# Performance work log

Measured on AMD Instinct MI355X. Metric: run time of the kernel, lower is better.

Reference implementation:

```python
import jax, jax.numpy as jnp
import numpy as np
import math

NUM_HEADS = 16
HEAD_DIM = 64
D_MODEL = NUM_HEADS * HEAD_DIM  # 1024
B, S = 4, 2048

def setup_inputs() -> dict:
    key = jax.random.key(0)
    ks = jax.random.split(key, 8)
    sd = 1.0 / math.sqrt(D_MODEL)
    return {
        "hidden_states": jax.random.normal(ks[0], (B, S, D_MODEL), jnp.float32),
        "attention_mask": jnp.zeros((B, 1, 1, S), jnp.float32),
        "Wq": jax.random.normal(ks[1], (D_MODEL, D_MODEL), jnp.float32) * sd,
        "bq": jnp.zeros((D_MODEL,), jnp.float32),
        "Wk": jax.random.normal(ks[2], (D_MODEL, D_MODEL), jnp.float32) * sd,
        "bk": jnp.zeros((D_MODEL,), jnp.float32),
        "Wv": jax.random.normal(ks[3], (D_MODEL, D_MODEL), jnp.float32) * sd,
        "bv": jnp.zeros((D_MODEL,), jnp.float32),
    }

def _split_heads(x):
    # [B, S, D] -> [B, H, S, hd]
    b, s, _ = x.shape
    return x.reshape(b, s, NUM_HEADS, HEAD_DIM).transpose(0, 2, 1, 3)

def reference(hidden_states, attention_mask, Wq, bq, Wk, bk, Wv, bv):
    # Linear projections (torch nn.Linear: x @ W.T + b)
    q = _split_heads(hidden_states @ Wq.T + bq)
    k = _split_heads(hidden_states @ Wk.T + bk)
    v = _split_heads(hidden_states @ Wv.T + bv)
    scale = 1.0 / math.sqrt(HEAD_DIM)
    # [B, H, Sq, Sk] attention scores, fully materialized as in the original
    scores = jnp.einsum("bhqd,bhkd->bhqk", q, k) * scale + attention_mask
    # relusq replacement for softmax
    probs = jnp.square(jax.nn.relu(scores))
    ctx = jnp.einsum("bhqk,bhkd->bhqd", probs, v)  # [B, H, S, hd]
    b = ctx.shape[0]
    return ctx.transpose(0, 2, 1, 3).reshape(b, -1, D_MODEL)
```

## Files before the change

### kernel.cpp

```cpp
#include <hip/hip_runtime.h>


typedef __bf16 bf16x8 __attribute__((ext_vector_type(8)));
typedef __bf16 bf16x4 __attribute__((ext_vector_type(4)));
typedef __bf16 bf16x2 __attribute__((ext_vector_type(2)));
typedef short  s16x4  __attribute__((ext_vector_type(4)));
typedef float  f32x4  __attribute__((ext_vector_type(4)));
typedef float  f32x16 __attribute__((ext_vector_type(16)));
typedef float  floatx4 __attribute__((ext_vector_type(4)));
typedef unsigned u32x2 __attribute__((ext_vector_type(2)));
typedef unsigned u32x4 __attribute__((ext_vector_type(4)));

#define MFMA16(a, b, c) __builtin_amdgcn_mfma_f32_16x16x32_bf16(a, b, c, 0, 0, 0)
#define MFMA32(a, b, c) __builtin_amdgcn_mfma_f32_32x32x16_bf16(a, b, c, 0, 0, 0)

#define WAITCNT_VM0() __builtin_amdgcn_s_waitcnt(0x0F70)
#define BARRIER() __builtin_amdgcn_s_barrier()
#define SETPRIO(p) __builtin_amdgcn_s_setprio(p)

__device__ __forceinline__ void glds16(const __bf16* g, __bf16* l) {
    __builtin_amdgcn_global_load_lds(
        (const __attribute__((address_space(1))) void*)g,
        (__attribute__((address_space(3))) void*)l, 16, 0, 0);
}

__global__ __launch_bounds__(256) void convert_kernel(
    const float* __restrict__ X, const float* __restrict__ Wq,
    const float* __restrict__ Wk, const float* __restrict__ Wv,
    __bf16* __restrict__ Xb, __bf16* __restrict__ Wqb,
    __bf16* __restrict__ Wkb, __bf16* __restrict__ Wvb)
{
    int blk = blockIdx.x;
    const float* src; __bf16* dst; size_t base;
    if (blk < 4096)      { src = X;  dst = Xb;  base = (size_t)blk * 2048; }
    else if (blk < 4608) { src = Wq; dst = Wqb; base = (size_t)(blk - 4096) * 2048; }
    else if (blk < 5120) { src = Wk; dst = Wkb; base = (size_t)(blk - 4608) * 2048; }
    else                 { src = Wv; dst = Wvb; base = (size_t)(blk - 5120) * 2048; }
    size_t off = base + (size_t)threadIdx.x * 8;
    floatx4 a = *(const floatx4*)(src + off);
    floatx4 c = *(const floatx4*)(src + off + 4);
    bf16x8 o;
    o[0] = (__bf16)a[0]; o[1] = (__bf16)a[1]; o[2] = (__bf16)a[2]; o[3] = (__bf16)a[3];
    o[4] = (__bf16)c[0]; o[5] = (__bf16)c[1]; o[6] = (__bf16)c[2]; o[7] = (__bf16)c[3];
    *(bf16x8*)(dst + off) = o;
}

__global__ __launch_bounds__(256) void qkv_gemm_kernel(
    const __bf16* __restrict__ Xb,
    const __bf16* __restrict__ Wqb, const __bf16* __restrict__ Wkb,
    const __bf16* __restrict__ Wvb,
    const float* __restrict__ bq, const float* __restrict__ bk,
    const float* __restrict__ bv,
    __bf16* __restrict__ qws, __bf16* __restrict__ kws, __bf16* __restrict__ vws)
{
    __shared__ __bf16 As[2][128 * 64];
    __shared__ __bf16 Bs[2][128 * 64];

    const int tid  = threadIdx.x;
    const int lane = tid & 63;
    const int wave = tid >> 6;
    const int wm   = (wave >> 1) * 64;
    const int wn   = (wave & 1) * 64;
    const int quad = lane >> 4;
    const int l16  = lane & 15;
    const int m0   = blockIdx.y * 128;

    const int sel = blockIdx.x >> 3;
    const bool vmode = (sel == 2);
    const __bf16* Wb = (sel == 0) ? Wqb : (sel == 1) ? Wkb : Wvb;
    const float* bias = (sel == 0) ? bq : (sel == 1) ? bk : bv;
    __bf16* outp = (sel == 0) ? qws : (sel == 1) ? kws : vws;
    const int n0 = (blockIdx.x & 7) * 128;

    const int woffA = vmode ? wm : wn;
    const int woffB = vmode ? wn : wm;

    const int srow = lane >> 3;
    const int schk = lane & 7;

    f32x4 acc[4][4] = {};

    #pragma unroll
    for (int i = 0; i < 4; ++i) {
        int rb = wave * 32 + i * 8;
        int r  = rb + srow;
        int c  = schk ^ (r & 7);
        glds16(Xb + (size_t)(m0 + r) * 1024 + c * 8, &As[0][rb * 64]);
        glds16(Wb + (size_t)(n0 + r) * 1024 + c * 8, &Bs[0][rb * 64]);
    }
    WAITCNT_VM0();
    BARRIER();

    for (int s = 0; s < 16; ++s) {
        const int kn = ((s + 1) & 15) * 64;
        const int nb = (s + 1) & 1;
        const int bc = s & 1;
        #pragma unroll
        for (int i = 0; i < 4; ++i) {
            int rb = wave * 32 + i * 8;
            int r  = rb + srow;
            int c  = schk ^ (r & 7);
            glds16(Xb + (size_t)(m0 + r) * 1024 + kn + c * 8, &As[nb][rb * 64]);
            glds16(Wb + (size_t)(n0 + r) * 1024 + kn + c * 8, &Bs[nb][rb * 64]);
        }

        const __bf16* Pa_ = vmode ? &As[bc][0] : &Bs[bc][0];
        const __bf16* Pb_ = vmode ? &Bs[bc][0] : &As[bc][0];

        SETPRIO(1);
        #pragma unroll
        for (int kk8 = 0; kk8 < 8; kk8 += 4) {
            bf16x8 af[4], bfr[4];
            #pragma unroll
            for (int a = 0; a < 4; ++a)
                af[a] = *(const bf16x8*)&Pa_[(woffA + a * 16 + l16) * 64 +
                                             (((kk8 + quad) ^ (l16 & 7)) * 8)];
            #pragma unroll
            for (int bb = 0; bb < 4; ++bb)
                bfr[bb] = *(const bf16x8*)&Pb_[(woffB + bb * 16 + l16) * 64 +
                                               (((kk8 + quad) ^ (l16 & 7)) * 8)];
            #pragma unroll
            for (int a = 0; a < 4; ++a)
                #pragma unroll
                for (int bb = 0; bb < 4; ++bb)
                    acc[a][bb] = MFMA16(af[a], bfr[bb], acc[a][bb]);
        }
        SETPRIO(0);

        WAITCNT_VM0();
        BARRIER();
    }

    if (!vmode) {
        #pragma unroll
        for (int a = 0; a < 4; ++a) {
            int n = n0 + woffA + a * 16 + quad * 4;
            floatx4 bv4 = *(const floatx4*)&bias[n];
            int h = n >> 6, d0 = n & 63;
            #pragma unroll
            for (int bb = 0; bb < 4; ++bb) {
                int m = m0 + woffB + bb * 16 + l16;
                int bt = m >> 11, ss = m & 2047;
                bf16x4 o;
                #pragma unroll
                for (int r = 0; r < 4; ++r)
                    o[r] = (__bf16)(acc[a][bb][r] + bv4[r]);
                *(bf16x4*)&outp[((size_t)(bt * 16 + h) * 2048 + ss) * 64 + d0] = o;
            }
        }
    } else {
        #pragma unroll
        for (int a = 0; a < 4; ++a) {
            int m = m0 + woffA + a * 16 + quad * 4;
            int bt = m >> 11, s0 = m & 2047;
            #pragma unroll
            for (int bb = 0; bb < 4; ++bb) {
                int n = n0 + woffB + bb * 16 + l16;
                float bvv = bias[n];
                int h = n >> 6, d = n & 63;
                bf16x4 o;
                #pragma unroll
                for (int r = 0; r < 4; ++r)
                    o[r] = (__bf16)(acc[a][bb][r] + bvv);
                *(bf16x4*)&outp[((size_t)(bt * 16 + h) * 64 + d) * 2048 + s0] = o;
            }
        }
    }
}

__global__ __launch_bounds__(512, 4) void attn_kernel(
    const __bf16* __restrict__ Q, const __bf16* __restrict__ K,
    const __bf16* __restrict__ Vt, const float* __restrict__ mask,
    float* __restrict__ out)
{
    __shared__ __bf16 Ks[2][2][64 * 64];
    __shared__ __bf16 Vs[2][2][64 * 64];
    __shared__ float  Ms[2048];

    const int tid  = threadIdx.x;
    const int lane = tid & 63;
    const int wave = tid >> 6;
    const int l32  = lane & 31;
    const int hi   = lane >> 5;
    const int bh   = blockIdx.x;
    const int b    = bh >> 4;
    const int h    = bh & 15;
    const int q0w  = blockIdx.y * 256 + wave * 32;

    const __bf16* Qb = Q  + (size_t)bh * 2048 * 64;
    const __bf16* Kb = K  + (size_t)bh * 2048 * 64;
    const __bf16* Vb = Vt + (size_t)bh * 64 * 2048;
    const float*  mb = mask + b * 2048;

    const int rb = wave * 8;
    const int sr = rb + (lane >> 3);
    const int sc = ((lane & 7) ^ (sr & 7)) * 8;

    bf16x8 aq[4];
    #pragma unroll
    for (int dk = 0; dk < 4; ++dk)
        aq[dk] = *(const bf16x8*)(Qb +
            (size_t)(q0w + l32) * 64 + dk * 16 + hi * 8);

    f32x16 co0 = {}, co1 = {};

    glds16(Kb + (size_t)sr * 64 + sc,        &Ks[0][0][rb * 64]);
    glds16(Kb + (size_t)(64 + sr) * 64 + sc, &Ks[0][1][rb * 64]);
    glds16(Vb + (size_t)sr * 2048 + sc,      &Vs[0][0][rb * 64]);
    glds16(Vb + (size_t)sr * 2048 + 64 + sc, &Vs[0][1][rb * 64]);
    glds16((const __bf16*)mb + (size_t)wave * 512 + lane * 8,
           (__bf16*)Ms + wave * 512);
    WAITCNT_VM0();
    BARRIER();

    for (int t = 0; t < 16; ++t) {
        const int kn = ((t + 1) & 15) * 128;
        const int nb = (t + 1) & 1;
        const int cb = t & 1;
        glds16(Kb + (size_t)(kn + sr) * 64 + sc,       &Ks[nb][0][rb * 64]);
        glds16(Kb + (size_t)(kn + 64 + sr) * 64 + sc,  &Ks[nb][1][rb * 64]);
        glds16(Vb + (size_t)sr * 2048 + kn + sc,       &Vs[nb][0][rb * 64]);
        glds16(Vb + (size_t)sr * 2048 + kn + 64 + sc,  &Vs[nb][1][rb * 64]);

        #pragma unroll
        for (int hf = 0; hf < 2; ++hf) {
            const __bf16* Kt = &Ks[cb][hf][0];
            const __bf16* Vtl = &Vs[cb][hf][0];
            const int k0 = t * 128 + hf * 64;

            f32x16 st0 = {}, st1 = {};
            SETPRIO(1);
            #pragma unroll
            for (int dk = 0; dk < 4; ++dk) {
                const int g = dk * 2 + hi;
                const int c0 = (g ^ (l32 & 7)) * 8;
                bf16x8 ak0 = *(const bf16x8*)&Kt[l32 * 64 + c0];
                bf16x8 ak1 = *(const bf16x8*)&Kt[(32 + l32) * 64 + c0];
                st0 = MFMA32(ak0, aq[dk], st0);
                st1 = MFMA32(ak1, aq[dk], st1);
            }
            SETPRIO(0);

            #pragma unroll
            for (int kg = 0; kg < 2; ++kg) {
                const f32x16 s = kg ? st1 : st0;
                const f32x4 zero4 = {};
                unsigned W[4][2];
                #pragma unroll
                for (int G = 0; G < 4; ++G) {
                    f32x4 v;
                    v[0] = s[G * 4 + 0]; v[1] = s[G * 4 + 1];
                    v[2] = s[G * 4 + 2]; v[3] = s[G * 4 + 3];
                    f32x4 mk = *(const f32x4*)&Ms[k0 + kg * 32 + G * 8 + hi * 4];
                    v = v * 0.125f + mk;
                    v = __builtin_elementwise_max(v, zero4);
                    v = v * v;
                    bf16x2 w0, w1;
                    w0[0] = (__bf16)v[0]; w0[1] = (__bf16)v[1];
                    w1[0] = (__bf16)v[2]; w1[1] = (__bf16)v[3];
                    W[G][0] = __builtin_bit_cast(unsigned, w0);
                    W[G][1] = __builtin_bit_cast(unsigned, w1);
                }
                u32x2 s00 = __builtin_amdgcn_permlane32_swap(W[0][0], W[1][0], false, false);
                u32x2 s01 = __builtin_amdgcn_permlane32_swap(W[0][1], W[1][1], false, false);
                u32x2 s10 = __builtin_amdgcn_permlane32_swap(W[2][0], W[3][0], false, false);
                u32x2 s11 = __builtin_amdgcn_permlane32_swap(W[2][1], W[3][1], false, false);
                u32x4 f0, f1;
                f0[0] = s00[0]; f0[1] = s01[0]; f0[2] = s00[1]; f0[3] = s01[1];
                f1[0] = s10[0]; f1[1] = s11[0]; f1[2] = s10[1]; f1[3] = s11[1];
                bf16x8 pa0 = __builtin_bit_cast(bf16x8, f0);
                bf16x8 pa1 = __builtin_bit_cast(bf16x8, f1);

                SETPRIO(1);
                #pragma unroll
                for (int dt = 0; dt < 2; ++dt) {
                    const int d = dt * 32 + l32;
                    const int ch0 = (kg * 4 + hi) ^ (d & 7);
                    const int ch1 = (kg * 4 + 2 + hi) ^ (d & 7);
                    bf16x8 vb0 = *(const bf16x8*)&Vtl[d * 64 + ch0 * 8];
                    bf16x8 vb1 = *(const bf16x8*)&Vtl[d * 64 + ch1 * 8];
                    if (dt == 0) {
                        co0 = MFMA32(pa0, vb0, co0);
                        co0 = MFMA32(pa1, vb1, co0);
                    } else {
                        co1 = MFMA32(pa0, vb0, co1);
                        co1 = MFMA32(pa1, vb1, co1);
                    }
                }
                SETPRIO(0);
            }
        }

        WAITCNT_VM0();
        BARRIER();
    }

    #pragma unroll
    for (int r = 0; r < 16; ++r) {
        int q = q0w + (r & 3) + 8 * (r >> 2) + 4 * hi;
        float* orow = &out[(((size_t)b * 2048 + q) * 16 + h) * 64];
        orow[l32]      = co0[r];
        orow[32 + l32] = co1[r];
    }
}

extern "C" void kernel_launch(void* const* d_in, const int* in_sizes, int n_in,
                              void* d_out, int out_size, void* d_ws, size_t ws_size,
                              hipStream_t stream) {
    const float* hidden = (const float*)d_in[0];
    const float* mask   = (const float*)d_in[1];
    const float* Wq     = (const float*)d_in[2];
    const float* bq     = (const float*)d_in[3];
    const float* Wk     = (const float*)d_in[4];
    const float* bk     = (const float*)d_in[5];
    const float* Wv     = (const float*)d_in[6];
    const float* bv     = (const float*)d_in[7];
    float* out = (float*)d_out;

    __bf16* qws = (__bf16*)d_ws;
    __bf16* kws = qws + (size_t)64 * 2048 * 64;
    __bf16* vws = kws + (size_t)64 * 2048 * 64;
    __bf16* Xb  = vws + (size_t)64 * 2048 * 64;
    __bf16* Wqb = Xb  + (size_t)8192 * 1024;
    __bf16* Wkb = Wqb + (size_t)1024 * 1024;
    __bf16* Wvb = Wkb + (size_t)1024 * 1024;

    convert_kernel<<<dim3(5632), dim3(256), 0, stream>>>(hidden, Wq, Wk, Wv,
                                                         Xb, Wqb, Wkb, Wvb);
    qkv_gemm_kernel<<<dim3(24, 64), dim3(256), 0, stream>>>(Xb, Wqb, Wkb, Wvb,
                                                            bq, bk, bv,
                                                            qws, kws, vws);
    attn_kernel<<<dim3(64, 8), dim3(512), 0, stream>>>(qws, kws, vws, mask, out);
}
```

Measured before the change: 241.3 us.

## Shrink attention blocks to 4 waves with 64-key tiles and more blocks

The attention kernel now uses 256-thread blocks covering 128 queries, and processes keys in 64-wide tiles over 32 iterations instead of 128-wide tiles over 16. Launching 1024 blocks instead of 512 and using half the shared memory for K/V buffers is meant to improve occupancy and load balance across CUs. In exchange, each K/V tile is reused by fewer query waves, so global/L2 traffic for K and V doubles, and there are twice as many barriers per block.

After: 241.0 us. Within noise of the previous version (-0.1%).

```diff
diff --git a/kernel.cpp b/kernel.cpp
--- a/kernel.cpp
+++ b/kernel.cpp
@@ -168,13 +168,13 @@
     }
 }
 
-__global__ __launch_bounds__(512, 4) void attn_kernel(
+__global__ __launch_bounds__(256, 4) void attn_kernel(
     const __bf16* __restrict__ Q, const __bf16* __restrict__ K,
     const __bf16* __restrict__ Vt, const float* __restrict__ mask,
     float* __restrict__ out)
 {
-    __shared__ __bf16 Ks[2][2][64 * 64];
-    __shared__ __bf16 Vs[2][2][64 * 64];
+    __shared__ __bf16 Ks[2][64 * 64];
+    __shared__ __bf16 Vs[2][64 * 64];
     __shared__ float  Ms[2048];
 
     const int tid  = threadIdx.x;
@@ -185,14 +185,14 @@
     const int bh   = blockIdx.x;
     const int b    = bh >> 4;
     const int h    = bh & 15;
-    const int q0w  = blockIdx.y * 256 + wave * 32;
+    const int q0w  = blockIdx.y * 128 + wave * 32;
 
     const __bf16* Qb = Q  + (size_t)bh * 2048 * 64;
     const __bf16* Kb = K  + (size_t)bh * 2048 * 64;
     const __bf16* Vb = Vt + (size_t)bh * 64 * 2048;
     const float*  mb = mask + b * 2048;
 
-    const int rb = wave * 8;
+    const int rb = wave * 16;
     const int sr = rb + (lane >> 3);
     const int sc = ((lane & 7) ^ (sr & 7)) * 8;
 
@@ -204,91 +204,90 @@
 
     f32x16 co0 = {}, co1 = {};
 
-    glds16(Kb + (size_t)sr * 64 + sc,        &Ks[0][0][rb * 64]);
-    glds16(Kb + (size_t)(64 + sr) * 64 + sc, &Ks[0][1][rb * 64]);
-    glds16(Vb + (size_t)sr * 2048 + sc,      &Vs[0][0][rb * 64]);
-    glds16(Vb + (size_t)sr * 2048 + 64 + sc, &Vs[0][1][rb * 64]);
-    glds16((const __bf16*)mb + (size_t)wave * 512 + lane * 8,
-           (__bf16*)Ms + wave * 512);
+    glds16(Kb + (size_t)sr * 64 + sc,            &Ks[0][rb * 64]);
+    glds16(Kb + (size_t)(sr + 8) * 64 + sc,      &Ks[0][(rb + 8) * 64]);
+    glds16(Vb + (size_t)sr * 2048 + sc,          &Vs[0][rb * 64]);
+    glds16(Vb + (size_t)(sr + 8) * 2048 + sc,    &Vs[0][(rb + 8) * 64]);
+    glds16((const __bf16*)mb + (size_t)(wave * 2) * 512 + lane * 8,
+           (__bf16*)Ms + (wave * 2) * 512);
+    glds16((const __bf16*)mb + (size_t)(wave * 2 + 1) * 512 + lane * 8,
+           (__bf16*)Ms + (wave * 2 + 1) * 512);
     WAITCNT_VM0();
     BARRIER();
 
-    for (int t = 0; t < 16; ++t) {
-        const int kn = ((t + 1) & 15) * 128;
+    for (int t = 0; t < 32; ++t) {
+        const int kn = ((t + 1) & 31) * 64;
         const int nb = (t + 1) & 1;
         const int cb = t & 1;
-        glds16(Kb + (size_t)(kn + sr) * 64 + sc,       &Ks[nb][0][rb * 64]);
-        glds16(Kb + (size_t)(kn + 64 + sr) * 64 + sc,  &Ks[nb][1][rb * 64]);
-        glds16(Vb + (size_t)sr * 2048 + kn + sc,       &Vs[nb][0][rb * 64]);
-        glds16(Vb + (size_t)sr * 2048 + kn + 64 + sc,  &Vs[nb][1][rb * 64]);
-
-        #pragma unroll
-        for (int hf = 0; hf < 2; ++hf) {
-            const __bf16* Kt = &Ks[cb][hf][0];
-            const __bf16* Vtl = &Vs[cb][hf][0];
-            const int k0 = t * 128 + hf * 64;
-
-            f32x16 st0 = {}, st1 = {};
+        glds16(Kb + (size_t)(kn + sr) * 64 + sc,         &Ks[nb][rb * 64]);
+        glds16(Kb + (size_t)(kn + sr + 8) * 64 + sc,     &Ks[nb][(rb + 8) * 64]);
+        glds16(Vb + (size_t)sr * 2048 + kn + sc,         &Vs[nb][rb * 64]);
+        glds16(Vb + (size_t)(sr + 8) * 2048 + kn + sc,   &Vs[nb][(rb + 8) * 64]);
+
+        const __bf16* Kt = &Ks[cb][0];
+        const __bf16* Vtl = &Vs[cb][0];
+        const int k0 = t * 64;
+
+        f32x16 st0 = {}, st1 = {};
+        SETPRIO(1);
+        #pragma unroll
+        for (int dk = 0; dk < 4; ++dk) {
+            const int g = dk * 2 + hi;
+            const int c0 = (g ^ (l32 & 7)) * 8;
+            bf16x8 ak0 = *(const bf16x8*)&Kt[l32 * 64 + c0];
+            bf16x8 ak1 = *(const bf16x8*)&Kt[(32 + l32) * 64 + c0];
+            st0 = MFMA32(ak0, aq[dk], st0);
+            st1 = MFMA32(ak1, aq[dk], st1);
+        }
+        SETPRIO(0);
+
+        #pragma unroll
+        for (int kg = 0; kg < 2; ++kg) {
+            const f32x16 s = kg ? st1 : st0;
+            const f32x4 zero4 = {};
+            unsigned W[4][2];
+            #pragma unroll
+            for (int G = 0; G < 4; ++G) {
+                f32x4 v;
+                v[0] = s[G * 4 + 0]; v[1] = s[G * 4 + 1];
+                v[2] = s[G * 4 + 2]; v[3] = s[G * 4 + 3];
+                f32x4 mk = *(const f32x4*)&Ms[k0 + kg * 32 + G * 8 + hi * 4];
+                v = v * 0.125f + mk;
+                v = __builtin_elementwise_max(v, zero4);
+                v = v * v;
+                bf16x2 w0, w1;
+                w0[0] = (__bf16)v[0]; w0[1] = (__bf16)v[1];
+                w1[0] = (__bf16)v[2]; w1[1] = (__bf16)v[3];
+                W[G][0] = __builtin_bit_cast(unsigned, w0);
+                W[G][1] = __builtin_bit_cast(unsigned, w1);
+            }
+            u32x2 s00 = __builtin_amdgcn_permlane32_swap(W[0][0], W[1][0], false, false);
+            u32x2 s01 = __builtin_amdgcn_permlane32_swap(W[0][1], W[1][1], false, false);
+            u32x2 s10 = __builtin_amdgcn_permlane32_swap(W[2][0], W[3][0], false, false);
+            u32x2 s11 = __builtin_amdgcn_permlane32_swap(W[2][1], W[3][1], false, false);
+            u32x4 f0, f1;
+            f0[0] = s00[0]; f0[1] = s01[0]; f0[2] = s00[1]; f0[3] = s01[1];
+            f1[0] = s10[0]; f1[1] = s11[0]; f1[2] = s10[1]; f1[3] = s11[1];
+            bf16x8 pa0 = __builtin_bit_cast(bf16x8, f0);
+            bf16x8 pa1 = __builtin_bit_cast(bf16x8, f1);
+
             SETPRIO(1);
             #pragma unroll
-            for (int dk = 0; dk < 4; ++dk) {
-                const int g = dk * 2 + hi;
-                const int c0 = (g ^ (l32 & 7)) * 8;
-                bf16x8 ak0 = *(const bf16x8*)&Kt[l32 * 64 + c0];
-                bf16x8 ak1 = *(const bf16x8*)&Kt[(32 + l32) * 64 + c0];
-                st0 = MFMA32(ak0, aq[dk], st0);
-                st1 = MFMA32(ak1, aq[dk], st1);
+            for (int dt = 0; dt < 2; ++dt) {
+                const int d = dt * 32 + l32;
+                const int ch0 = (kg * 4 + hi) ^ (d & 7);
+                const int ch1 = (kg * 4 + 2 + hi) ^ (d & 7);
+                bf16x8 vb0 = *(const bf16x8*)&Vtl[d * 64 + ch0 * 8];
+                bf16x8 vb1 = *(const bf16x8*)&Vtl[d * 64 + ch1 * 8];
+                if (dt == 0) {
+                    co0 = MFMA32(pa0, vb0, co0);
+                    co0 = MFMA32(pa1, vb1, co0);
+                } else {
+                    co1 = MFMA32(pa0, vb0, co1);
+                    co1 = MFMA32(pa1, vb1, co1);
+                }
             }
             SETPRIO(0);
-
-            #pragma unroll
-            for (int kg = 0; kg < 2; ++kg) {
-                const f32x16 s = kg ? st1 : st0;
-                const f32x4 zero4 = {};
-                unsigned W[4][2];
-                #pragma unroll
-                for (int G = 0; G < 4; ++G) {
-                    f32x4 v;
-                    v[0] = s[G * 4 + 0]; v[1] = s[G * 4 + 1];
-                    v[2] = s[G * 4 + 2]; v[3] = s[G * 4 + 3];
-                    f32x4 mk = *(const f32x4*)&Ms[k0 + kg * 32 + G * 8 + hi * 4];
-                    v = v * 0.125f + mk;
-                    v = __builtin_elementwise_max(v, zero4);
-                    v = v * v;
-                    bf16x2 w0, w1;
-                    w0[0] = (__bf16)v[0]; w0[1] = (__bf16)v[1];
-                    w1[0] = (__bf16)v[2]; w1[1] = (__bf16)v[3];
-                    W[G][0] = __builtin_bit_cast(unsigned, w0);
-                    W[G][1] = __builtin_bit_cast(unsigned, w1);
-                }
-                u32x2 s00 = __builtin_amdgcn_permlane32_swap(W[0][0], W[1][0], false, false);
-                u32x2 s01 = __builtin_amdgcn_permlane32_swap(W[0][1], W[1][1], false, false);
-                u32x2 s10 = __builtin_amdgcn_permlane32_swap(W[2][0], W[3][0], false, false);
-                u32x2 s11 = __builtin_amdgcn_permlane32_swap(W[2][1], W[3][1], false, false);
-                u32x4 f0, f1;
-                f0[0] = s00[0]; f0[1] = s01[0]; f0[2] = s00[1]; f0[3] = s01[1];
-                f1[0] = s10[0]; f1[1] = s11[0]; f1[2] = s10[1]; f1[3] = s11[1];
-                bf16x8 pa0 = __builtin_bit_cast(bf16x8, f0);
-                bf16x8 pa1 = __builtin_bit_cast(bf16x8, f1);
-
-                SETPRIO(1);
-                #pragma unroll
-                for (int dt = 0; dt < 2; ++dt) {
-                    const int d = dt * 32 + l32;
-                    const int ch0 = (kg * 4 + hi) ^ (d & 7);
-                    const int ch1 = (kg * 4 + 2 + hi) ^ (d & 7);
-                    bf16x8 vb0 = *(const bf16x8*)&Vtl[d * 64 + ch0 * 8];
-                    bf16x8 vb1 = *(const bf16x8*)&Vtl[d * 64 + ch1 * 8];
-                    if (dt == 0) {
-                        co0 = MFMA32(pa0, vb0, co0);
-                        co0 = MFMA32(pa1, vb1, co0);
-                    } else {
-                        co1 = MFMA32(pa0, vb0, co1);
-                        co1 = MFMA32(pa1, vb1, co1);
-                    }
-                }
-                SETPRIO(0);
-            }
         }
 
         WAITCNT_VM0();
@@ -330,5 +329,5 @@
     qkv_gemm_kernel<<<dim3(24, 64), dim3(256), 0, stream>>>(Xb, Wqb, Wkb, Wvb,
                                                             bq, bk, bv,
                                                             qws, kws, vws);
-    attn_kernel<<<dim3(64, 8), dim3(512), 0, stream>>>(qws, kws, vws, mask, out);
-}
+    attn_kernel<<<dim3(64, 16), dim3(256), 0, stream>>>(qws, kws, vws, mask, out);
+}
```

## Enlarge QKV GEMM tile to 256x128 with 8 waves and triple-buffered LDS pipeline

Applied to the files above, without the earlier changes.

The QKV projection GEMM now uses 512-thread blocks computing 256x128 tiles, so each loaded weight tile is reused across twice as many rows. It also switches to a three-stage LDS ring that prefetches two K-steps ahead. Global-to-LDS loads are interleaved between the two MFMA phases, with partial vmcnt waits and extra barriers. This aims to hide load latency and improve data reuse. The cost is more LDS per block (about 144KB), fewer blocks in the grid, and more barriers per iteration.

Measured after the change: 240.9 us. About the same (-0.2%).

```diff
diff --git a/kernel.cpp b/kernel.cpp
--- a/kernel.cpp
+++ b/kernel.cpp
@@ -15,6 +15,7 @@
 #define MFMA32(a, b, c) __builtin_amdgcn_mfma_f32_32x32x16_bf16(a, b, c, 0, 0, 0)
 
 #define WAITCNT_VM0() __builtin_amdgcn_s_waitcnt(0x0F70)
+#define WAITCNT_VM6() __builtin_amdgcn_s_waitcnt(0x0F76)
 #define BARRIER() __builtin_amdgcn_s_barrier()
 #define SETPRIO(p) __builtin_amdgcn_s_setprio(p)
 
@@ -45,7 +46,7 @@
     *(bf16x8*)(dst + off) = o;
 }
 
-__global__ __launch_bounds__(256) void qkv_gemm_kernel(
+__global__ __launch_bounds__(512, 2) void qkv_gemm_kernel(
     const __bf16* __restrict__ Xb,
     const __bf16* __restrict__ Wqb, const __bf16* __restrict__ Wkb,
     const __bf16* __restrict__ Wvb,
@@ -53,17 +54,15 @@
     const float* __restrict__ bv,
     __bf16* __restrict__ qws, __bf16* __restrict__ kws, __bf16* __restrict__ vws)
 {
-    __shared__ __bf16 As[2][128 * 64];
-    __shared__ __bf16 Bs[2][128 * 64];
+    __shared__ __bf16 As[3][256 * 64];
+    __shared__ __bf16 Bs[3][128 * 64];
 
     const int tid  = threadIdx.x;
     const int lane = tid & 63;
     const int wave = tid >> 6;
-    const int wm   = (wave >> 1) * 64;
-    const int wn   = (wave & 1) * 64;
     const int quad = lane >> 4;
     const int l16  = lane & 15;
-    const int m0   = blockIdx.y * 128;
+    const int m0   = blockIdx.y * 256;
 
     const int sel = blockIdx.x >> 3;
     const bool vmode = (sel == 2);
@@ -72,74 +71,84 @@
     __bf16* outp = (sel == 0) ? qws : (sel == 1) ? kws : vws;
     const int n0 = (blockIdx.x & 7) * 128;
 
-    const int woffA = vmode ? wm : wn;
-    const int woffB = vmode ? wn : wm;
+    const int wA = vmode ? (wave & 3) * 64 : (wave >> 2) * 64;
+    const int wB = vmode ? (wave >> 2) * 64 : (wave & 3) * 64;
 
     const int srow = lane >> 3;
     const int schk = lane & 7;
 
     f32x4 acc[4][4] = {};
 
-    #pragma unroll
-    for (int i = 0; i < 4; ++i) {
-        int rb = wave * 32 + i * 8;
-        int r  = rb + srow;
-        int c  = schk ^ (r & 7);
-        glds16(Xb + (size_t)(m0 + r) * 1024 + c * 8, &As[0][rb * 64]);
-        glds16(Wb + (size_t)(n0 + r) * 1024 + c * 8, &Bs[0][rb * 64]);
-    }
-    WAITCNT_VM0();
+#define QKV_STAGE_A(bb, kt, i) { \
+        int rb_ = wave * 32 + (i) * 8; int r_ = rb_ + srow; \
+        int c_ = schk ^ (r_ & 7); \
+        glds16(Xb + (size_t)(m0 + r_) * 1024 + (kt) * 64 + c_ * 8, \
+               &As[bb][rb_ * 64]); }
+#define QKV_STAGE_B(bb, kt, i) { \
+        int rb_ = wave * 16 + (i) * 8; int r_ = rb_ + srow; \
+        int c_ = schk ^ (r_ & 7); \
+        glds16(Wb + (size_t)(n0 + r_) * 1024 + (kt) * 64 + c_ * 8, \
+               &Bs[bb][rb_ * 64]); }
+
+    #pragma unroll
+    for (int i = 0; i < 4; ++i) QKV_STAGE_A(0, 0, i);
+    #pragma unroll
+    for (int i = 0; i < 2; ++i) QKV_STAGE_B(0, 0, i);
+    #pragma unroll
+    for (int i = 0; i < 4; ++i) QKV_STAGE_A(1, 1, i);
+    #pragma unroll
+    for (int i = 0; i < 2; ++i) QKV_STAGE_B(1, 1, i);
+    WAITCNT_VM6();
     BARRIER();
 
     for (int s = 0; s < 16; ++s) {
-        const int kn = ((s + 1) & 15) * 64;
-        const int nb = (s + 1) & 1;
-        const int bc = s & 1;
+        const int cb  = s % 3;
+        const int pb  = (s + 2) % 3;
+        const int kt2 = (s + 2) & 15;
+        const __bf16* Pa_ = vmode ? &As[cb][0] : &Bs[cb][0];
+        const __bf16* Pb_ = vmode ? &Bs[cb][0] : &As[cb][0];
+
         #pragma unroll
-        for (int i = 0; i < 4; ++i) {
-            int rb = wave * 32 + i * 8;
-            int r  = rb + srow;
-            int c  = schk ^ (r & 7);
-            glds16(Xb + (size_t)(m0 + r) * 1024 + kn + c * 8, &As[nb][rb * 64]);
-            glds16(Wb + (size_t)(n0 + r) * 1024 + kn + c * 8, &Bs[nb][rb * 64]);
-        }
-
-        const __bf16* Pa_ = vmode ? &As[bc][0] : &Bs[bc][0];
-        const __bf16* Pb_ = vmode ? &Bs[bc][0] : &As[bc][0];
-
-        SETPRIO(1);
-        #pragma unroll
-        for (int kk8 = 0; kk8 < 8; kk8 += 4) {
+        for (int p = 0; p < 2; ++p) {
             bf16x8 af[4], bfr[4];
             #pragma unroll
             for (int a = 0; a < 4; ++a)
-                af[a] = *(const bf16x8*)&Pa_[(woffA + a * 16 + l16) * 64 +
-                                             (((kk8 + quad) ^ (l16 & 7)) * 8)];
+                af[a] = *(const bf16x8*)&Pa_[(wA + a * 16 + l16) * 64 +
+                                             (((p * 4 + quad) ^ (l16 & 7)) * 8)];
             #pragma unroll
             for (int bb = 0; bb < 4; ++bb)
-                bfr[bb] = *(const bf16x8*)&Pb_[(woffB + bb * 16 + l16) * 64 +
-                                               (((kk8 + quad) ^ (l16 & 7)) * 8)];
+                bfr[bb] = *(const bf16x8*)&Pb_[(wB + bb * 16 + l16) * 64 +
+                                               (((p * 4 + quad) ^ (l16 & 7)) * 8)];
+            QKV_STAGE_A(pb, kt2, 2 * p);
+            QKV_STAGE_A(pb, kt2, 2 * p + 1);
+            QKV_STAGE_B(pb, kt2, p);
+
+            if (p == 1) WAITCNT_VM6();
+            BARRIER();
+
+            SETPRIO(1);
             #pragma unroll
             for (int a = 0; a < 4; ++a)
                 #pragma unroll
                 for (int bb = 0; bb < 4; ++bb)
                     acc[a][bb] = MFMA16(af[a], bfr[bb], acc[a][bb]);
+            SETPRIO(0);
+            BARRIER();
         }
-        SETPRIO(0);
-
-        WAITCNT_VM0();
-        BARRIER();
     }
+
+#undef QKV_STAGE_A
+#undef QKV_STAGE_B
 
     if (!vmode) {
         #pragma unroll
         for (int a = 0; a < 4; ++a) {
-            int n = n0 + woffA + a * 16 + quad * 4;
+            int n = n0 + wA + a * 16 + quad * 4;
             floatx4 bv4 = *(const floatx4*)&bias[n];
             int h = n >> 6, d0 = n & 63;
             #pragma unroll
             for (int bb = 0; bb < 4; ++bb) {
-                int m = m0 + woffB + bb * 16 + l16;
+                int m = m0 + wB + bb * 16 + l16;
                 int bt = m >> 11, ss = m & 2047;
                 bf16x4 o;
                 #pragma unroll
@@ -151,11 +160,11 @@
     } else {
         #pragma unroll
         for (int a = 0; a < 4; ++a) {
-            int m = m0 + woffA + a * 16 + quad * 4;
+            int m = m0 + wA + a * 16 + quad * 4;
             int bt = m >> 11, s0 = m & 2047;
             #pragma unroll
             for (int bb = 0; bb < 4; ++bb) {
-                int n = n0 + woffB + bb * 16 + l16;
+                int n = n0 + wB + bb * 16 + l16;
                 float bvv = bias[n];
                 int h = n >> 6, d = n & 63;
                 bf16x4 o;
@@ -327,7 +336,7 @@
 
     convert_kernel<<<dim3(5632), dim3(256), 0, stream>>>(hidden, Wq, Wk, Wv,
                                                          Xb, Wqb, Wkb, Wvb);
-    qkv_gemm_kernel<<<dim3(24, 64), dim3(256), 0, stream>>>(Xb, Wqb, Wkb, Wvb,
+    qkv_gemm_kernel<<<dim3(24, 32), dim3(512), 0, stream>>>(Xb, Wqb, Wkb, Wvb,
                                                             bq, bk, bv,
                                                             qws, kws, vws);
     attn_kernel<<<dim3(64, 8), dim3(512), 0, stream>>>(qws, kws, vws, mask, out);
```
